# Kernel tuning notes

Hardware: AMD Instinct MI355X
Metric: run time of the kernel (lower is better)

Reference implementation:

```python
import jax, jax.numpy as jnp
import numpy as np

B_GRAPHS, N_NODES = 16, 4096
IN_CH, HID = 256, 512
HEADS, HC = 1, 512  # SGFormerAttention(hidden, heads=1, head_channels=hidden)
NUM_LAYERS = 2
LN_EPS = 1e-5
QK_EPS = 1e-6


def setup_inputs() -> dict:
    key = jax.random.key(0)
    ks = jax.random.split(key, 10)

    def w(k, shape, scale=0.02):
        return jax.random.normal(k, shape, jnp.float32) * scale

    inp = {
        "x": jax.random.normal(ks[0], (B_GRAPHS * N_NODES, IN_CH), jnp.float32),
        "fc0_w": w(ks[1], (HID, IN_CH)),
        "fc0_b": jnp.zeros((HID,), jnp.float32),
        "ln0_g": jnp.ones((HID,), jnp.float32),
        "ln0_b": jnp.zeros((HID,), jnp.float32),
        "q0_w": w(ks[2], (HEADS * HC, HID)),
        "k0_w": w(ks[3], (HEADS * HC, HID)),
        "v0_w": w(ks[4], (HEADS * HC, HID)),
        "ln1_g": jnp.ones((HID,), jnp.float32),
        "ln1_b": jnp.zeros((HID,), jnp.float32),
        "q1_w": w(ks[5], (HEADS * HC, HID)),
        "k1_w": w(ks[6], (HEADS * HC, HID)),
        "v1_w": w(ks[7], (HEADS * HC, HID)),
        "ln2_g": jnp.ones((HID,), jnp.float32),
        "ln2_b": jnp.zeros((HID,), jnp.float32),
        "batch": jnp.repeat(jnp.arange(B_GRAPHS, dtype=jnp.int32), N_NODES),
        "num_graphs": B_GRAPHS,
    }
    return inp


def layernorm(x, g, b):
    mu = x.mean(axis=-1, keepdims=True)
    var = ((x - mu) ** 2).mean(axis=-1, keepdims=True)
    return (x - mu) / jnp.sqrt(var + LN_EPS) * g + b


def sg_attention(x, qw, kw, vw):
    # x: [B, N, HID]; linear (kernelized) global attention, softmax-free.
    B, N, _ = x.shape
    q = (x @ qw.T).reshape(B, N, HEADS, HC)
    k = (x @ kw.T).reshape(B, N, HEADS, HC)
    v = (x @ vw.T).reshape(B, N, HEADS, HC)
    q = jnp.where(q == 0, QK_EPS, q)
    k = jnp.where(k == 0, QK_EPS, k)
    q = q / jnp.linalg.norm(q, axis=-1, keepdims=True)
    k = k / jnp.linalg.norm(k, axis=-1, keepdims=True)
    kvs = jnp.einsum('blhm,blhd->bhmd', k, v)          # [B,H,HC,HC]
    num = jnp.einsum('bnhm,bhmd->bnhd', q, kvs) + N * v
    ks_sum = k.sum(axis=1)                             # [B,H,HC]
    denom = jnp.einsum('bnhm,bhm->bnh', q, ks_sum)[..., None] + float(N)
    return (num / denom).mean(axis=2)                  # [B,N,HC] (mean over heads)


def reference(x, fc0_w, fc0_b, ln0_g, ln0_b,
              q0_w, k0_w, v0_w, ln1_g, ln1_b,
              q1_w, k1_w, v1_w, ln2_g, ln2_b,
              batch, num_graphs):
    total = x.shape[0]
    # stable sort by graph id, remember inverse permutation
    indices = jnp.argsort(batch, stable=True)
    rev_perm = jnp.zeros((total,), jnp.int32).at[indices].set(
        jnp.arange(total, dtype=jnp.int32))
    xs = x[indices]
    # uniform graph sizes -> to_dense_batch is a reshape; mask is all-True
    h = xs.reshape(num_graphs, total // num_graphs, x.shape[1])
    h = h @ fc0_w.T + fc0_b
    h = jax.nn.relu(layernorm(h, ln0_g, ln0_b))  # dropout inactive (eval)
    layers = [h]
    for (qw, kw, vw, g, b) in ((q0_w, k0_w, v0_w, ln1_g, ln1_b),
                               (q1_w, k1_w, v1_w, ln2_g, ln2_b)):
        a = sg_attention(layers[-1], qw, kw, vw)
        a = (a + layers[-1]) / 2.0
        a = jax.nn.relu(layernorm(a, g, b))
        layers.append(a)
    out = layers[-1].reshape(total, -1)
    return out[rev_perm]
```

## Files before the change

kernel.cpp:

```cpp
#include <hip/hip_runtime.h>

#define TNODES 65536
#define NGRAPH 16
#define NNODE  4096
#define INCH   256
#define HID    512

using u16 = unsigned short;
using u32 = unsigned int;
using v8s = __attribute__((ext_vector_type(8))) short;
using v4f = __attribute__((ext_vector_type(4))) float;

__device__ __forceinline__ float bf2f(u16 u) {
    union { u32 i; float f; } v; v.i = ((u32)u) << 16; return v.f;
}
__device__ __forceinline__ u16 f2bf(float f) {
    union { float f; u32 i; } v; v.f = f;
    u32 x = v.i;
    return (u16)((x + 0x7fffu + ((x >> 16) & 1u)) >> 16);
}
__device__ __forceinline__ void up4(uint2 p, float* f) {
    f[0] = __uint_as_float(p.x << 16); f[1] = __uint_as_float(p.x & 0xffff0000u);
    f[2] = __uint_as_float(p.y << 16); f[3] = __uint_as_float(p.y & 0xffff0000u);
}
__device__ __forceinline__ uint2 pk4(float a, float b, float c, float d) {
    uint2 r;
    r.x = (u32)f2bf(a) | ((u32)f2bf(b) << 16);
    r.y = (u32)f2bf(c) | ((u32)f2bf(d) << 16);
    return r;
}

#define MFMA(a, b, c) __builtin_amdgcn_mfma_f32_16x16x32_bf16((a), (b), (c), 0, 0, 0)

#define GLD16(gp, sp) __builtin_amdgcn_global_load_lds( \
    (const __attribute__((address_space(1))) u32*)(const void*)(gp), \
    (__attribute__((address_space(3))) u32*)(void*)(sp), 16, 0, 0)

#define CFENCE() asm volatile("" ::: "memory")

__global__ void k_cvt4(const float* __restrict__ s, u16* __restrict__ d, int n4) {
    for (int i = blockIdx.x * blockDim.x + threadIdx.x; i < n4; i += gridDim.x * blockDim.x) {
        float4 f = ((const float4*)s)[i];
        ((uint2*)d)[i] = pk4(f.x, f.y, f.z, f.w);
    }
}

__global__ void k_zero(float* __restrict__ p, int n) {
    int i = blockIdx.x * 256 + threadIdx.x;
    if (i < n) p[i] = 0.f;
}

__global__ void k_red4(const u16* __restrict__ p, u16* __restrict__ o, int n8) {
    const size_t P = (size_t)NGRAPH * HID * HID;
    for (int i = blockIdx.x * blockDim.x + threadIdx.x; i < n8; i += gridDim.x * blockDim.x) {
        size_t b = (size_t)i * 8;
        float s[8] = {0.f, 0.f, 0.f, 0.f, 0.f, 0.f, 0.f, 0.f};
        #pragma unroll
        for (int ss = 0; ss < 4; ++ss) {
            v8s v = *(const v8s*)(p + ss * P + b);
            const u16* vp = (const u16*)&v;
            #pragma unroll
            for (int j = 0; j < 8; ++j) s[j] += bf2f(vp[j]);
        }
        uint2 lo = pk4(s[0], s[1], s[2], s[3]);
        uint2 hi = pk4(s[4], s[5], s[6], s[7]);
        uint4 w; w.x = lo.x; w.y = lo.y; w.z = hi.x; w.w = hi.y;
        *(uint4*)(o + b) = w;
    }
}

template<int LDK, int KLEN>
__device__ __forceinline__ void gemm_core(const u16* __restrict__ A,
                                          const u16* __restrict__ W,
                                          u16* sA, u16* sW, v4f (&acc)[8][2]) {
    const int t = threadIdx.x, lane = t & 63;
    const int q = lane >> 4, m15 = lane & 15;
    const int w = t >> 6, wr = w >> 2, wc = w & 3;

    #pragma unroll
    for (int n = 0; n < 8; ++n)
        #pragma unroll
        for (int rt = 0; rt < 2; ++rt)
            #pragma unroll
            for (int e = 0; e < 4; ++e) acc[n][rt][e] = 0.f;

    int aoff[2], woff[8];
    #pragma unroll
    for (int rt = 0; rt < 2; ++rt) {
        int r = wr * 32 + rt * 16 + m15;
        aoff[rt] = r * 32 + ((q ^ ((r >> 1) & 3)) * 8);
    }
    #pragma unroll
    for (int n = 0; n < 8; ++n) {
        int r = wc * 128 + n * 16 + m15;
        woff[n] = r * 32 + ((q ^ ((r >> 1) & 3)) * 8);
    }

    auto stage = [&](int k0, int buf) {
        u16* dW = sW + buf * (512 * 32);
        #pragma unroll
        for (int p = 0; p < 4; ++p) {
            int sf = p * 512 + t, row = sf >> 2, sl = sf & 3;
            int gc = k0 + ((sl ^ ((row >> 1) & 3)) * 8);
            GLD16(W + (size_t)row * LDK + gc, dW + sf * 8);
        }
        if (t < 256) {
            int row = t >> 2, sl = t & 3;
            int gc = k0 + ((sl ^ ((row >> 1) & 3)) * 8);
            GLD16(A + (size_t)row * LDK + gc, sA + buf * (64 * 32) + t * 8);
        }
    };

    const int KT = KLEN / 32;
    stage(0, 0);
    stage(32, 1);
    int cur = 0;
    const bool lowt = (t < 256);
    for (int kt = 0; kt < KT; ++kt) {
        if (kt + 1 < KT) {
            if (lowt) asm volatile("s_waitcnt vmcnt(5)" ::: "memory");
            else      asm volatile("s_waitcnt vmcnt(4)" ::: "memory");
        } else {
            asm volatile("s_waitcnt vmcnt(0)" ::: "memory");
        }
        __builtin_amdgcn_s_barrier();
        CFENCE();
        __builtin_amdgcn_sched_barrier(0);
        const u16* cA = sA + cur * (64 * 32);
        const u16* cW = sW + cur * (512 * 32);
        v8s b0 = *(const v8s*)(cA + aoff[0]);
        v8s b1 = *(const v8s*)(cA + aoff[1]);
        #pragma unroll
        for (int n = 0; n < 8; ++n) {
            v8s af = *(const v8s*)(cW + woff[n]);
            acc[n][0] = MFMA(af, b0, acc[n][0]);
            acc[n][1] = MFMA(af, b1, acc[n][1]);
        }
        CFENCE();
        __builtin_amdgcn_s_barrier();
        CFENCE();
        if (kt + 2 < KT) stage((kt + 2) * 32, cur);
        cur ^= 1;
    }
}


__device__ __forceinline__ int tswz(int c) {
    return (((c >> 2) & 3) << 4) ^ ((c & 3) << 3);
}

__launch_bounds__(512, 4)
__global__ void k_fc(const u16* __restrict__ xb, const u16* __restrict__ wb,
                     const float* __restrict__ bias, const float* __restrict__ lg,
                     const float* __restrict__ lb, u16* __restrict__ h) {
    __shared__ u16 sA[2][64 * 32];
    __shared__ u16 sW[2][512 * 32];
    __shared__ float red[2][64][4];
    __shared__ float rowv[2][64];
    const int t = threadIdx.x, lane = t & 63, w = t >> 6;
    const int q = lane >> 4, m15 = lane & 15;
    const int wr = w >> 2, wc = w & 3;
    const int bx = (int)blockIdx.x;
    const int swz = (bx & 7) * ((int)gridDim.x >> 3) + (bx >> 3);
    const int r0 = swz * 64;
    v4f acc[8][2];
    gemm_core<INCH, INCH>(xb + (size_t)r0 * INCH, wb, &sA[0][0], &sW[0][0], acc);

    float sm0 = 0.f, sm1 = 0.f, sq0 = 0.f, sq1 = 0.f;
    #pragma unroll
    for (int n = 0; n < 8; ++n) {
        int c = wc * 128 + n * 16 + q * 4;
        float4 bi = *(const float4*)(bias + c);
        const float* bp = &bi.x;
        #pragma unroll
        for (int rt = 0; rt < 2; ++rt)
            #pragma unroll
            for (int e = 0; e < 4; ++e) {
                float a = acc[n][rt][e] + bp[e];
                acc[n][rt][e] = a;
                if (rt == 0) { sm0 += a; sq0 += a * a; } else { sm1 += a; sq1 += a * a; }
            }
    }
    sm0 += __shfl_xor(sm0, 16); sm0 += __shfl_xor(sm0, 32);
    sq0 += __shfl_xor(sq0, 16); sq0 += __shfl_xor(sq0, 32);
    sm1 += __shfl_xor(sm1, 16); sm1 += __shfl_xor(sm1, 32);
    sq1 += __shfl_xor(sq1, 16); sq1 += __shfl_xor(sq1, 32);
    if (lane < 16) {
        red[0][wr * 32 + m15][wc] = sm0; red[0][wr * 32 + 16 + m15][wc] = sm1;
        red[1][wr * 32 + m15][wc] = sq0; red[1][wr * 32 + 16 + m15][wc] = sq1;
    }
    __syncthreads();
    if (t < 64) {
        float tt = red[0][t][0] + red[0][t][1] + red[0][t][2] + red[0][t][3];
        float t2 = red[1][t][0] + red[1][t][1] + red[1][t][2] + red[1][t][3];
        float mu = tt * (1.f / HID);
        float rs = rsqrtf(t2 * (1.f / HID) - mu * mu + 1e-5f);
        rowv[0][t] = mu; rowv[1][t] = rs;
    }
    __syncthreads();
    #pragma unroll
    for (int n = 0; n < 8; ++n) {
        int c = wc * 128 + n * 16 + q * 4;
        float4 g4 = *(const float4*)(lg + c);
        float4 b4 = *(const float4*)(lb + c);
        #pragma unroll
        for (int rt = 0; rt < 2; ++rt) {
            int row = wr * 32 + rt * 16 + m15;
            float mu = rowv[0][row], rs = rowv[1][row];
            float v0 = (acc[n][rt][0] - mu) * rs * g4.x + b4.x;
            float v1 = (acc[n][rt][1] - mu) * rs * g4.y + b4.y;
            float v2 = (acc[n][rt][2] - mu) * rs * g4.z + b4.z;
            float v3 = (acc[n][rt][3] - mu) * rs * g4.w + b4.w;
            v0 = v0 > 0.f ? v0 : 0.f; v1 = v1 > 0.f ? v1 : 0.f;
            v2 = v2 > 0.f ? v2 : 0.f; v3 = v3 > 0.f ? v3 : 0.f;
            *(uint2*)&h[(size_t)(r0 + row) * HID + c] = pk4(v0, v1, v2, v3);
        }
    }
}

__launch_bounds__(512, 4)
__global__ void k_proj(const u16* __restrict__ hsrc, const u16* __restrict__ wkb,
                       const u16* __restrict__ wvb, u16* __restrict__ kt,
                       u16* __restrict__ vt, float* __restrict__ vo,
                       float* __restrict__ ksum) {
    __shared__ char smem[8192 + 65536 + 1024 + 256];
    u16* sA = (u16*)smem;
    u16* sW = (u16*)(smem + 8192);
    u16* sT = sW;
    float (*red)[4] = (float(*)[4])(smem + 8192 + 65536);
    float* rowv = (float*)(smem + 8192 + 65536 + 1024);
    const int t = threadIdx.x, lane = t & 63, w = t >> 6;
    const int q = lane >> 4, m15 = lane & 15;
    const int wr = w >> 2, wc = w & 3;
    const int bx = (int)blockIdx.x;
    const int swz = (bx & 7) * ((int)gridDim.x >> 3) + (bx >> 3);
    const int r0 = swz * 64;
    const int g = swz >> 6;
    const int lbase = (swz & 63) * 64;
    const int mode = blockIdx.y;
    v4f acc[8][2];
    gemm_core<HID, HID>(hsrc + (size_t)r0 * HID, mode ? wvb : wkb,
                        sA, sW, acc);

    if (mode == 0) {
        float sq0 = 0.f, sq1 = 0.f;
        #pragma unroll
        for (int n = 0; n < 8; ++n)
            #pragma unroll
            for (int rt = 0; rt < 2; ++rt)
                #pragma unroll
                for (int e = 0; e < 4; ++e) {
                    float vv = acc[n][rt][e];
                    if (vv == 0.f) vv = 1e-6f;
                    acc[n][rt][e] = vv;
                    if (rt == 0) sq0 += vv * vv; else sq1 += vv * vv;
                }
        sq0 += __shfl_xor(sq0, 16); sq0 += __shfl_xor(sq0, 32);
        sq1 += __shfl_xor(sq1, 16); sq1 += __shfl_xor(sq1, 32);
        if (lane < 16) {
            red[wr * 32 + m15][wc] = sq0; red[wr * 32 + 16 + m15][wc] = sq1;
        }
        __syncthreads();
        if (t < 64)
            rowv[t] = rsqrtf(red[t][0] + red[t][1] + red[t][2] + red[t][3]);
        __syncthreads();
        #pragma unroll
        for (int n = 0; n < 8; ++n)
            #pragma unroll
            for (int rt = 0; rt < 2; ++rt) {
                int row = wr * 32 + rt * 16 + m15;
                float rn = rowv[row];
                #pragma unroll
                for (int e = 0; e < 4; ++e) {
                    int c = wc * 128 + n * 16 + q * 4 + e;
                    sT[(c << 6) + (row ^ tswz(c))] = f2bf(acc[n][rt][e] * rn);
                }
            }
        __syncthreads();
        const int ch = t;
        const int xs = (((ch >> 2) & 3) << 1) ^ (ch & 3);
        u16* op = kt + ((size_t)(g * 512 + ch)) * NNODE + lbase;
        float sum = 0.f;
        #pragma unroll
        for (int jj = 0; jj < 8; ++jj) {
            v8s cvec = *(const v8s*)&sT[(ch << 6) + jj * 8];
            int l0 = (jj ^ xs) * 8;
            *(v8s*)(op + l0) = cvec;
            const u16* cp = (const u16*)&cvec;
            #pragma unroll
            for (int i = 0; i < 8; ++i) sum += bf2f(cp[i]);
        }
        atomicAdd(&ksum[g * 512 + ch], sum);
    } else {
        #pragma unroll
        for (int n = 0; n < 8; ++n) {
            int c = wc * 128 + n * 16 + q * 4;
            #pragma unroll
            for (int rt = 0; rt < 2; ++rt) {
                int row = wr * 32 + rt * 16 + m15;
                float4 o = {acc[n][rt][0], acc[n][rt][1], acc[n][rt][2], acc[n][rt][3]};
                *(float4*)&vo[(size_t)(r0 + row) * HID + c] = o;
                #pragma unroll
                for (int e = 0; e < 4; ++e)
                    sT[((c + e) << 6) + (row ^ tswz(c + e))] = f2bf(acc[n][rt][e]);
            }
        }
        __syncthreads();
        const int ch = t;
        const int xs = (((ch >> 2) & 3) << 1) ^ (ch & 3);
        u16* op = vt + ((size_t)(g * 512 + ch)) * NNODE + lbase;
        #pragma unroll
        for (int jj = 0; jj < 8; ++jj) {
            v8s cvec = *(const v8s*)&sT[(ch << 6) + jj * 8];
            int l0 = (jj ^ xs) * 8;
            *(v8s*)(op + l0) = cvec;
        }
    }
}

__launch_bounds__(512, 4)
__global__ void k_kvmm2(const u16* __restrict__ kt, const u16* __restrict__ vt,
                        u16* __restrict__ kvp) {
    __shared__ u16 sA[2][64 * 32];
    __shared__ u16 sW[2][512 * 32];
    const int t = threadIdx.x, lane = t & 63, w = t >> 6;
    const int q = lane >> 4, m15 = lane & 15;
    const int wr = w >> 2, wc = w & 3;
    const int bx = (int)blockIdx.x;
    const int swz = (bx & 7) * 64 + (bx >> 3);
    const int db = swz & 7, s = (swz >> 3) & 3, g = swz >> 5;
    const u16* A = vt + ((size_t)(g * 512 + db * 64)) * NNODE + s * 1024;
    const u16* W = kt + ((size_t)(g * 512)) * NNODE + s * 1024;
    v4f acc[8][2];
    gemm_core<NNODE, 1024>(A, W, &sA[0][0], &sW[0][0], acc);
    u16* plane = kvp + (size_t)s * NGRAPH * HID * HID;
    #pragma unroll
    for (int n = 0; n < 8; ++n) {
        int m = wc * 128 + n * 16 + q * 4;
        #pragma unroll
        for (int rt = 0; rt < 2; ++rt) {
            int d = db * 64 + wr * 32 + rt * 16 + m15;
            *(uint2*)&plane[((size_t)(g * 512) + d) * 512 + m] =
                pk4(acc[n][rt][0], acc[n][rt][1], acc[n][rt][2], acc[n][rt][3]);
        }
    }
}

__launch_bounds__(512, 4)
__global__ void k_qnorm(const u16* __restrict__ hsrc, const u16* __restrict__ qwb,
                        const float* __restrict__ ks, u16* __restrict__ qo,
                        float* __restrict__ dnv) {
    __shared__ u16 sA[2][64 * 32];
    __shared__ u16 sW[2][512 * 32];
    __shared__ float red[2][64][4];
    __shared__ float rowv[64];
    const int t = threadIdx.x, lane = t & 63, w = t >> 6;
    const int q = lane >> 4, m15 = lane & 15;
    const int wr = w >> 2, wc = w & 3;
    const int bx = (int)blockIdx.x;
    const int swz = (bx & 7) * ((int)gridDim.x >> 3) + (bx >> 3);
    const int r0 = swz * 64;
    const int gi = swz >> 6;
    v4f acc[8][2];
    gemm_core<HID, HID>(hsrc + (size_t)r0 * HID, qwb, &sA[0][0], &sW[0][0], acc);

    float ss0 = 0.f, ss1 = 0.f, ws0 = 0.f, ws1 = 0.f;
    #pragma unroll
    for (int n = 0; n < 8; ++n) {
        int c = wc * 128 + n * 16 + q * 4;
        float4 kv = *(const float4*)(ks + (gi << 9) + c);
        const float* kp = &kv.x;
        #pragma unroll
        for (int rt = 0; rt < 2; ++rt)
            #pragma unroll
            for (int e = 0; e < 4; ++e) {
                float vv = acc[n][rt][e];
                if (vv == 0.f) vv = 1e-6f;
                acc[n][rt][e] = vv;
                if (rt == 0) { ss0 += vv * vv; ws0 += vv * kp[e]; }
                else         { ss1 += vv * vv; ws1 += vv * kp[e]; }
            }
    }
    ss0 += __shfl_xor(ss0, 16); ss0 += __shfl_xor(ss0, 32);
    ss1 += __shfl_xor(ss1, 16); ss1 += __shfl_xor(ss1, 32);
    ws0 += __shfl_xor(ws0, 16); ws0 += __shfl_xor(ws0, 32);
    ws1 += __shfl_xor(ws1, 16); ws1 += __shfl_xor(ws1, 32);
    if (lane < 16) {
        red[0][wr * 32 + m15][wc] = ss0; red[0][wr * 32 + 16 + m15][wc] = ss1;
        red[1][wr * 32 + m15][wc] = ws0; red[1][wr * 32 + 16 + m15][wc] = ws1;
    }
    __syncthreads();
    if (t < 64) {
        float st = red[0][t][0] + red[0][t][1] + red[0][t][2] + red[0][t][3];
        float wt = red[1][t][0] + red[1][t][1] + red[1][t][2] + red[1][t][3];
        float rn = rsqrtf(st);
        rowv[t] = rn;
        dnv[r0 + t] = 1.f / (rn * wt + (float)NNODE);
    }
    __syncthreads();
    #pragma unroll
    for (int n = 0; n < 8; ++n) {
        int c = wc * 128 + n * 16 + q * 4;
        #pragma unroll
        for (int rt = 0; rt < 2; ++rt) {
            int row = wr * 32 + rt * 16 + m15;
            float rn = rowv[row];
            *(uint2*)&qo[(size_t)(r0 + row) * HID + c] =
                pk4(acc[n][rt][0] * rn, acc[n][rt][1] * rn,
                    acc[n][rt][2] * rn, acc[n][rt][3] * rn);
        }
    }
}

__launch_bounds__(512, 4)
__global__ void k_attn2(const u16* __restrict__ qhat, const u16* __restrict__ kvstb,
                        const float* __restrict__ dnv, const float* __restrict__ vsrc,
                        const u16* __restrict__ hsrc, const float* __restrict__ lg,
                        const float* __restrict__ lb, u16* __restrict__ outb,
                        float* __restrict__ outf) {
    __shared__ u16 sA[2][64 * 32];
    __shared__ u16 sW[2][512 * 32];
    __shared__ float red[2][64][4];
    __shared__ float rowv[2][64];
    const int t = threadIdx.x, lane = t & 63, w = t >> 6;
    const int q = lane >> 4, m15 = lane & 15;
    const int wr = w >> 2, wc = w & 3;
    const int bx = (int)blockIdx.x;
    const int swz = (bx & 7) * ((int)gridDim.x >> 3) + (bx >> 3);
    const int r0 = swz * 64;
    const int gi = swz >> 6;
    v4f acc[8][2];
    gemm_core<HID, HID>(qhat + (size_t)r0 * HID, kvstb + (size_t)gi * HID * HID,
                        &sA[0][0], &sW[0][0], acc);

    const float dv0 = dnv[r0 + wr * 32 + m15];
    const float dv1 = dnv[r0 + wr * 32 + 16 + m15];
    float sm0 = 0.f, sm1 = 0.f, sq0 = 0.f, sq1 = 0.f;
    #pragma unroll
    for (int n = 0; n < 8; ++n) {
        int c = wc * 128 + n * 16 + q * 4;
        #pragma unroll
        for (int rt = 0; rt < 2; ++rt) {
            int row = wr * 32 + rt * 16 + m15;
            size_t og = (size_t)(r0 + row) * HID + c;
            float hh[4]; up4(*(const uint2*)&hsrc[og], hh);
            float4 vv = *(const float4*)&vsrc[og];
            const float* vp = &vv.x;
            float dv = rt ? dv1 : dv0;
            #pragma unroll
            for (int e = 0; e < 4; ++e) {
                float a = ((acc[n][rt][e] + (float)NNODE * vp[e]) * dv + hh[e]) * 0.5f;
                acc[n][rt][e] = a;
                if (rt == 0) { sm0 += a; sq0 += a * a; } else { sm1 += a; sq1 += a * a; }
            }
        }
    }
    sm0 += __shfl_xor(sm0, 16); sm0 += __shfl_xor(sm0, 32);
    sq0 += __shfl_xor(sq0, 16); sq0 += __shfl_xor(sq0, 32);
    sm1 += __shfl_xor(sm1, 16); sm1 += __shfl_xor(sm1, 32);
    sq1 += __shfl_xor(sq1, 16); sq1 += __shfl_xor(sq1, 32);
    if (lane < 16) {
        red[0][wr * 32 + m15][wc] = sm0; red[0][wr * 32 + 16 + m15][wc] = sm1;
        red[1][wr * 32 + m15][wc] = sq0; red[1][wr * 32 + 16 + m15][wc] = sq1;
    }
    __syncthreads();
    if (t < 64) {
        float tt = red[0][t][0] + red[0][t][1] + red[0][t][2] + red[0][t][3];
        float t2 = red[1][t][0] + red[1][t][1] + red[1][t][2] + red[1][t][3];
        float mu = tt * (1.f / HID);
        float rs = rsqrtf(t2 * (1.f / HID) - mu * mu + 1e-5f);
        rowv[0][t] = mu; rowv[1][t] = rs;
    }
    __syncthreads();
    #pragma unroll
    for (int n = 0; n < 8; ++n) {
        int c = wc * 128 + n * 16 + q * 4;
        float4 g4 = *(const float4*)(lg + c);
        float4 b4 = *(const float4*)(lb + c);
        #pragma unroll
        for (int rt = 0; rt < 2; ++rt) {
            int row = wr * 32 + rt * 16 + m15;
            float mu = rowv[0][row], rs = rowv[1][row];
            float v0 = (acc[n][rt][0] - mu) * rs * g4.x + b4.x;
            float v1 = (acc[n][rt][1] - mu) * rs * g4.y + b4.y;
            float v2 = (acc[n][rt][2] - mu) * rs * g4.z + b4.z;
            float v3 = (acc[n][rt][3] - mu) * rs * g4.w + b4.w;
            v0 = v0 > 0.f ? v0 : 0.f; v1 = v1 > 0.f ? v1 : 0.f;
            v2 = v2 > 0.f ? v2 : 0.f; v3 = v3 > 0.f ? v3 : 0.f;
            size_t og = (size_t)(r0 + row) * HID + c;
            if (outf) {
                float4 o = {v0, v1, v2, v3};
                *(float4*)&outf[og] = o;
            } else {
                *(uint2*)&outb[og] = pk4(v0, v1, v2, v3);
            }
        }
    }
}

extern "C" void kernel_launch(void* const* d_in, const int* in_sizes, int n_in,
                              void* d_out, int out_size, void* d_ws, size_t ws_size,
                              hipStream_t stream) {
    const float* x    = (const float*)d_in[0];
    const float* fc0w = (const float*)d_in[1];
    const float* fc0b = (const float*)d_in[2];
    const float* ln0g = (const float*)d_in[3];
    const float* ln0b = (const float*)d_in[4];
    const float* q0w  = (const float*)d_in[5];
    const float* k0w  = (const float*)d_in[6];
    const float* v0w  = (const float*)d_in[7];
    const float* ln1g = (const float*)d_in[8];
    const float* ln1b = (const float*)d_in[9];
    const float* q1w  = (const float*)d_in[10];
    const float* k1w  = (const float*)d_in[11];
    const float* v1w  = (const float*)d_in[12];
    const float* ln2g = (const float*)d_in[13];
    const float* ln2b = (const float*)d_in[14];

    const size_t M64 = (size_t)TNODES * HID * 2;
    const size_t PL  = (size_t)NGRAPH * HID * HID * 2;
    char* wsc = (char*)d_ws;
    u16*   H   = (u16*)wsc;
    u16*   Kt  = (u16*)(wsc + M64);
    u16*   Vt  = (u16*)(wsc + 2 * M64);
    u16*   KVp = (u16*)(wsc + 3 * M64);
    u16*   KVb = (u16*)(wsc + 3 * M64 + 4 * PL);
    float* KS  = (float*)(wsc + 3 * M64 + 5 * PL);
    float* DNV = KS + NGRAPH * HID;
    u16*   Wc  = (u16*)((char*)DNV + (size_t)TNODES * sizeof(float));
    u16* fc0wb = Wc;
    u16* q0b = Wc + 131072;
    u16* k0b = Wc + 393216;
    u16* v0b = Wc + 655360;
    u16* q1b = Wc + 917504;
    u16* k1b = Wc + 1179648;
    u16* v1b = Wc + 1441792;
    u16* Xb  = Vt;
    u16* QH  = Vt;
    float* V = (float*)d_out;

    dim3 b256(256), b512(512);
    k_cvt4<<<dim3(64),  b256, 0, stream>>>(fc0w, fc0wb, HID * INCH / 4);
    k_cvt4<<<dim3(64),  b256, 0, stream>>>(q0w, q0b, HID * HID / 4);
    k_cvt4<<<dim3(64),  b256, 0, stream>>>(k0w, k0b, HID * HID / 4);
    k_cvt4<<<dim3(64),  b256, 0, stream>>>(v0w, v0b, HID * HID / 4);
    k_cvt4<<<dim3(64),  b256, 0, stream>>>(q1w, q1b, HID * HID / 4);
    k_cvt4<<<dim3(64),  b256, 0, stream>>>(k1w, k1b, HID * HID / 4);
    k_cvt4<<<dim3(64),  b256, 0, stream>>>(v1w, v1b, HID * HID / 4);
    k_cvt4<<<dim3(1024), b256, 0, stream>>>(x, Xb, TNODES * INCH / 4);

    k_fc<<<dim3(TNODES / 64), b512, 0, stream>>>(Xb, fc0wb, fc0b, ln0g, ln0b, H);

    k_zero<<<dim3(32), b256, 0, stream>>>(KS, NGRAPH * HID);
    k_proj<<<dim3(TNODES / 64, 2), b512, 0, stream>>>(H, k0b, v0b, Kt, Vt, V, KS);
    k_kvmm2<<<dim3(512), b512, 0, stream>>>(Kt, Vt, KVp);
    k_red4<<<dim3(2048), b256, 0, stream>>>(KVp, KVb, NGRAPH * HID * HID / 8);
    k_qnorm<<<dim3(TNODES / 64), b512, 0, stream>>>(H, q0b, KS, QH, DNV);
    k_attn2<<<dim3(TNODES / 64), b512, 0, stream>>>(QH, KVb, DNV, V, H, ln1g, ln1b,
                                                    H, nullptr);

    k_zero<<<dim3(32), b256, 0, stream>>>(KS, NGRAPH * HID);
    k_proj<<<dim3(TNODES / 64, 2), b512, 0, stream>>>(H, k1b, v1b, Kt, Vt, V, KS);
    k_kvmm2<<<dim3(512), b512, 0, stream>>>(Kt, Vt, KVp);
    k_red4<<<dim3(2048), b256, 0, stream>>>(KVp, KVb, NGRAPH * HID * HID / 8);
    k_qnorm<<<dim3(TNODES / 64), b512, 0, stream>>>(H, q1b, KS, QH, DNV);
    k_attn2<<<dim3(TNODES / 64), b512, 0, stream>>>(QH, KVb, DNV, V, H, ln2g, ln2b,
                                                    nullptr, (float*)d_out);
}
```

Measured before the change: 1.095 ms.

## Enlarge GEMM row tile from 64 to 128 rows across all fused kernels

```diff
diff --git a/kernel.cpp b/kernel.cpp
--- a/kernel.cpp
+++ b/kernel.cpp
@@ -72,7 +72,7 @@
 template<int LDK, int KLEN>
 __device__ __forceinline__ void gemm_core(const u16* __restrict__ A,
                                           const u16* __restrict__ W,
-                                          u16* sA, u16* sW, v4f (&acc)[8][2]) {
+                                          u16* sA, u16* sW, v4f (&acc)[8][4]) {
     const int t = threadIdx.x, lane = t & 63;
     const int q = lane >> 4, m15 = lane & 15;
     const int w = t >> 6, wr = w >> 2, wc = w & 3;
@@ -80,14 +80,14 @@
     #pragma unroll
     for (int n = 0; n < 8; ++n)
         #pragma unroll
-        for (int rt = 0; rt < 2; ++rt)
+        for (int rt = 0; rt < 4; ++rt)
             #pragma unroll
             for (int e = 0; e < 4; ++e) acc[n][rt][e] = 0.f;
 
-    int aoff[2], woff[8];
-    #pragma unroll
-    for (int rt = 0; rt < 2; ++rt) {
-        int r = wr * 32 + rt * 16 + m15;
+    int aoff[4], woff[8];
+    #pragma unroll
+    for (int rt = 0; rt < 4; ++rt) {
+        int r = wr * 64 + rt * 16 + m15;
         aoff[rt] = r * 32 + ((q ^ ((r >> 1) & 3)) * 8);
     }
     #pragma unroll
@@ -104,10 +104,10 @@
             int gc = k0 + ((sl ^ ((row >> 1) & 3)) * 8);
             GLD16(W + (size_t)row * LDK + gc, dW + sf * 8);
         }
-        if (t < 256) {
+        {
             int row = t >> 2, sl = t & 3;
             int gc = k0 + ((sl ^ ((row >> 1) & 3)) * 8);
-            GLD16(A + (size_t)row * LDK + gc, sA + buf * (64 * 32) + t * 8);
+            GLD16(A + (size_t)row * LDK + gc, sA + buf * (128 * 32) + t * 8);
         }
     };
 
@@ -115,26 +115,23 @@
     stage(0, 0);
     stage(32, 1);
     int cur = 0;
-    const bool lowt = (t < 256);
     for (int kt = 0; kt < KT; ++kt) {
-        if (kt + 1 < KT) {
-            if (lowt) asm volatile("s_waitcnt vmcnt(5)" ::: "memory");
-            else      asm volatile("s_waitcnt vmcnt(4)" ::: "memory");
-        } else {
-            asm volatile("s_waitcnt vmcnt(0)" ::: "memory");
-        }
+        if (kt + 1 < KT) asm volatile("s_waitcnt vmcnt(5)" ::: "memory");
+        else             asm volatile("s_waitcnt vmcnt(0)" ::: "memory");
         __builtin_amdgcn_s_barrier();
         CFENCE();
         __builtin_amdgcn_sched_barrier(0);
-        const u16* cA = sA + cur * (64 * 32);
+        const u16* cA = sA + cur * (128 * 32);
         const u16* cW = sW + cur * (512 * 32);
-        v8s b0 = *(const v8s*)(cA + aoff[0]);
-        v8s b1 = *(const v8s*)(cA + aoff[1]);
+        v8s b[4];
+        #pragma unroll
+        for (int rt = 0; rt < 4; ++rt) b[rt] = *(const v8s*)(cA + aoff[rt]);
         #pragma unroll
         for (int n = 0; n < 8; ++n) {
             v8s af = *(const v8s*)(cW + woff[n]);
-            acc[n][0] = MFMA(af, b0, acc[n][0]);
-            acc[n][1] = MFMA(af, b1, acc[n][1]);
+            #pragma unroll
+            for (int rt = 0; rt < 4; ++rt)
+                acc[n][rt] = MFMA(af, b[rt], acc[n][rt]);
         }
         CFENCE();
         __builtin_amdgcn_s_barrier();
@@ -149,48 +146,51 @@
     return (((c >> 2) & 3) << 4) ^ ((c & 3) << 3);
 }
 
-__launch_bounds__(512, 4)
+__launch_bounds__(512, 2)
 __global__ void k_fc(const u16* __restrict__ xb, const u16* __restrict__ wb,
                      const float* __restrict__ bias, const float* __restrict__ lg,
                      const float* __restrict__ lb, u16* __restrict__ h) {
-    __shared__ u16 sA[2][64 * 32];
+    __shared__ u16 sA[2][128 * 32];
     __shared__ u16 sW[2][512 * 32];
-    __shared__ float red[2][64][4];
-    __shared__ float rowv[2][64];
+    __shared__ float red[2][128][4];
+    __shared__ float rowv[2][128];
     const int t = threadIdx.x, lane = t & 63, w = t >> 6;
     const int q = lane >> 4, m15 = lane & 15;
     const int wr = w >> 2, wc = w & 3;
     const int bx = (int)blockIdx.x;
     const int swz = (bx & 7) * ((int)gridDim.x >> 3) + (bx >> 3);
-    const int r0 = swz * 64;
-    v4f acc[8][2];
+    const int r0 = swz * 128;
+    v4f acc[8][4];
     gemm_core<INCH, INCH>(xb + (size_t)r0 * INCH, wb, &sA[0][0], &sW[0][0], acc);
 
-    float sm0 = 0.f, sm1 = 0.f, sq0 = 0.f, sq1 = 0.f;
+    float sm[4] = {0.f, 0.f, 0.f, 0.f}, sq[4] = {0.f, 0.f, 0.f, 0.f};
     #pragma unroll
     for (int n = 0; n < 8; ++n) {
         int c = wc * 128 + n * 16 + q * 4;
         float4 bi = *(const float4*)(bias + c);
         const float* bp = &bi.x;
         #pragma unroll
-        for (int rt = 0; rt < 2; ++rt)
+        for (int rt = 0; rt < 4; ++rt)
             #pragma unroll
             for (int e = 0; e < 4; ++e) {
                 float a = acc[n][rt][e] + bp[e];
                 acc[n][rt][e] = a;
-                if (rt == 0) { sm0 += a; sq0 += a * a; } else { sm1 += a; sq1 += a * a; }
-            }
-    }
-    sm0 += __shfl_xor(sm0, 16); sm0 += __shfl_xor(sm0, 32);
-    sq0 += __shfl_xor(sq0, 16); sq0 += __shfl_xor(sq0, 32);
-    sm1 += __shfl_xor(sm1, 16); sm1 += __shfl_xor(sm1, 32);
-    sq1 += __shfl_xor(sq1, 16); sq1 += __shfl_xor(sq1, 32);
-    if (lane < 16) {
-        red[0][wr * 32 + m15][wc] = sm0; red[0][wr * 32 + 16 + m15][wc] = sm1;
-        red[1][wr * 32 + m15][wc] = sq0; red[1][wr * 32 + 16 + m15][wc] = sq1;
-    }
+                sm[rt] += a; sq[rt] += a * a;
+            }
+    }
+    #pragma unroll
+    for (int rt = 0; rt < 4; ++rt) {
+        sm[rt] += __shfl_xor(sm[rt], 16); sm[rt] += __shfl_xor(sm[rt], 32);
+        sq[rt] += __shfl_xor(sq[rt], 16); sq[rt] += __shfl_xor(sq[rt], 32);
+    }
+    if (lane < 16)
+        #pragma unroll
+        for (int rt = 0; rt < 4; ++rt) {
+            red[0][wr * 64 + rt * 16 + m15][wc] = sm[rt];
+            red[1][wr * 64 + rt * 16 + m15][wc] = sq[rt];
+        }
     __syncthreads();
-    if (t < 64) {
+    if (t < 128) {
         float tt = red[0][t][0] + red[0][t][1] + red[0][t][2] + red[0][t][3];
         float t2 = red[1][t][0] + red[1][t][1] + red[1][t][2] + red[1][t][3];
         float mu = tt * (1.f / HID);
@@ -204,8 +204,8 @@
         float4 g4 = *(const float4*)(lg + c);
         float4 b4 = *(const float4*)(lb + c);
         #pragma unroll
-        for (int rt = 0; rt < 2; ++rt) {
-            int row = wr * 32 + rt * 16 + m15;
+        for (int rt = 0; rt < 4; ++rt) {
+            int row = wr * 64 + rt * 16 + m15;
             float mu = rowv[0][row], rs = rowv[1][row];
             float v0 = (acc[n][rt][0] - mu) * rs * g4.x + b4.x;
             float v1 = (acc[n][rt][1] - mu) * rs * g4.y + b4.y;
@@ -218,77 +218,85 @@
     }
 }
 
-__launch_bounds__(512, 4)
+__launch_bounds__(512, 2)
 __global__ void k_proj(const u16* __restrict__ hsrc, const u16* __restrict__ wkb,
                        const u16* __restrict__ wvb, u16* __restrict__ kt,
                        u16* __restrict__ vt, float* __restrict__ vo,
                        float* __restrict__ ksum) {
-    __shared__ char smem[8192 + 65536 + 1024 + 256];
-    u16* sA = (u16*)smem;
-    u16* sW = (u16*)(smem + 8192);
-    u16* sT = sW;
-    float (*red)[4] = (float(*)[4])(smem + 8192 + 65536);
-    float* rowv = (float*)(smem + 8192 + 65536 + 1024);
+    __shared__ u16 sA[2][128 * 32];
+    __shared__ u16 sW[2][512 * 32];
+    __shared__ float red[128][4];
+    __shared__ float rowv[128];
+    u16* sT = &sW[0][0];
     const int t = threadIdx.x, lane = t & 63, w = t >> 6;
     const int q = lane >> 4, m15 = lane & 15;
     const int wr = w >> 2, wc = w & 3;
     const int bx = (int)blockIdx.x;
     const int swz = (bx & 7) * ((int)gridDim.x >> 3) + (bx >> 3);
-    const int r0 = swz * 64;
-    const int g = swz >> 6;
-    const int lbase = (swz & 63) * 64;
+    const int r0 = swz * 128;
+    const int g = swz >> 5;
+    const int lbase = (swz & 31) * 128;
     const int mode = blockIdx.y;
-    v4f acc[8][2];
+    v4f acc[8][4];
     gemm_core<HID, HID>(hsrc + (size_t)r0 * HID, mode ? wvb : wkb,
-                        sA, sW, acc);
-
+                        &sA[0][0], &sW[0][0], acc);
+
+    const int ch = t;
+    const int xs = (((ch >> 2) & 3) << 1) ^ (ch & 3);
     if (mode == 0) {
-        float sq0 = 0.f, sq1 = 0.f;
+        float sq[4] = {0.f, 0.f, 0.f, 0.f};
         #pragma unroll
         for (int n = 0; n < 8; ++n)
             #pragma unroll
-            for (int rt = 0; rt < 2; ++rt)
+            for (int rt = 0; rt < 4; ++rt)
                 #pragma unroll
                 for (int e = 0; e < 4; ++e) {
                     float vv = acc[n][rt][e];
                     if (vv == 0.f) vv = 1e-6f;
                     acc[n][rt][e] = vv;
-                    if (rt == 0) sq0 += vv * vv; else sq1 += vv * vv;
+                    sq[rt] += vv * vv;
                 }
-        sq0 += __shfl_xor(sq0, 16); sq0 += __shfl_xor(sq0, 32);
-        sq1 += __shfl_xor(sq1, 16); sq1 += __shfl_xor(sq1, 32);
-        if (lane < 16) {
-            red[wr * 32 + m15][wc] = sq0; red[wr * 32 + 16 + m15][wc] = sq1;
-        }
+        #pragma unroll
+        for (int rt = 0; rt < 4; ++rt) {
+            sq[rt] += __shfl_xor(sq[rt], 16); sq[rt] += __shfl_xor(sq[rt], 32);
+        }
+        if (lane < 16)
+            #pragma unroll
+            for (int rt = 0; rt < 4; ++rt)
+                red[wr * 64 + rt * 16 + m15][wc] = sq[rt];
         __syncthreads();
-        if (t < 64)
+        if (t < 128)
             rowv[t] = rsqrtf(red[t][0] + red[t][1] + red[t][2] + red[t][3]);
         __syncthreads();
-        #pragma unroll
-        for (int n = 0; n < 8; ++n)
-            #pragma unroll
-            for (int rt = 0; rt < 2; ++rt) {
-                int row = wr * 32 + rt * 16 + m15;
-                float rn = rowv[row];
+        float sum = 0.f;
+        #pragma unroll
+        for (int pass = 0; pass < 2; ++pass) {
+            if (wr == pass) {
                 #pragma unroll
-                for (int e = 0; e < 4; ++e) {
-                    int c = wc * 128 + n * 16 + q * 4 + e;
-                    sT[(c << 6) + (row ^ tswz(c))] = f2bf(acc[n][rt][e] * rn);
-                }
-            }
-        __syncthreads();
-        const int ch = t;
-        const int xs = (((ch >> 2) & 3) << 1) ^ (ch & 3);
-        u16* op = kt + ((size_t)(g * 512 + ch)) * NNODE + lbase;
-        float sum = 0.f;
-        #pragma unroll
-        for (int jj = 0; jj < 8; ++jj) {
-            v8s cvec = *(const v8s*)&sT[(ch << 6) + jj * 8];
-            int l0 = (jj ^ xs) * 8;
-            *(v8s*)(op + l0) = cvec;
-            const u16* cp = (const u16*)&cvec;
-            #pragma unroll
-            for (int i = 0; i < 8; ++i) sum += bf2f(cp[i]);
+                for (int n = 0; n < 8; ++n)
+                    #pragma unroll
+                    for (int rt = 0; rt < 4; ++rt) {
+                        int rl = rt * 16 + m15;
+                        float rn = rowv[wr * 64 + rl];
+                        #pragma unroll
+                        for (int e = 0; e < 4; ++e) {
+                            int c = wc * 128 + n * 16 + q * 4 + e;
+                            sT[(c << 6) + (rl ^ tswz(c))] = f2bf(acc[n][rt][e] * rn);
+                        }
+                    }
+            }
+            __syncthreads();
+            u16* op = kt + ((size_t)(g * 512 + ch)) * NNODE + lbase + pass * 64;
+            #pragma unroll
+            for (int jj = 0; jj < 8; ++jj) {
+                v8s cvec = *(const v8s*)&sT[(ch << 6) + jj * 8];
+                int l0 = (jj ^ xs) * 8;
+                *(v8s*)(op + l0) = cvec;
+                const u16* cp = (const u16*)&cvec;
+                #pragma unroll
+                for (int i = 0; i < 8; ++i) sum += bf2f(cp[i]);
+            }
+            __syncthreads();
         }
         atomicAdd(&ksum[g * 512 + ch], sum);
     } else {
@@ -296,101 +304,115 @@
         for (int n = 0; n < 8; ++n) {
             int c = wc * 128 + n * 16 + q * 4;
             #pragma unroll
-            for (int rt = 0; rt < 2; ++rt) {
-                int row = wr * 32 + rt * 16 + m15;
+            for (int rt = 0; rt < 4; ++rt) {
+                int row = wr * 64 + rt * 16 + m15;
                 float4 o = {acc[n][rt][0], acc[n][rt][1], acc[n][rt][2], acc[n][rt][3]};
                 *(float4*)&vo[(size_t)(r0 + row) * HID + c] = o;
+            }
+        }
+        #pragma unroll
+        for (int pass = 0; pass < 2; ++pass) {
+            if (wr == pass) {
                 #pragma unroll
-                for (int e = 0; e < 4; ++e)
-                    sT[((c + e) << 6) + (row ^ tswz(c + e))] = f2bf(acc[n][rt][e]);
-            }
-        }
-        __syncthreads();
-        const int ch = t;
-        const int xs = (((ch >> 2) & 3) << 1) ^ (ch & 3);
-        u16* op = vt + ((size_t)(g * 512 + ch)) * NNODE + lbase;
-        #pragma unroll
-        for (int jj = 0; jj < 8; ++jj) {
-            v8s cvec = *(const v8s*)&sT[(ch << 6) + jj * 8];
-            int l0 = (jj ^ xs) * 8;
-            *(v8s*)(op + l0) = cvec;
-        }
-    }
-}
-
-__launch_bounds__(512, 4)
+                for (int n = 0; n < 8; ++n)
+                    #pragma unroll
+                    for (int rt = 0; rt < 4; ++rt) {
+                        int rl = rt * 16 + m15;
+                        #pragma unroll
+                        for (int e = 0; e < 4; ++e) {
+                            int c = wc * 128 + n * 16 + q * 4 + e;
+                            sT[(c << 6) + (rl ^ tswz(c))] = f2bf(acc[n][rt][e]);
+                        }
+                    }
+            }
+            __syncthreads();
+            u16* op = vt + ((size_t)(g * 512 + ch)) * NNODE + lbase + pass * 64;
+            #pragma unroll
+            for (int jj = 0; jj < 8; ++jj) {
+                v8s cvec = *(const v8s*)&sT[(ch << 6) + jj * 8];
+                int l0 = (jj ^ xs) * 8;
+                *(v8s*)(op + l0) = cvec;
+            }
+            __syncthreads();
+        }
+    }
+}
+
+__launch_bounds__(512, 2)
 __global__ void k_kvmm2(const u16* __restrict__ kt, const u16* __restrict__ vt,
                         u16* __restrict__ kvp) {
-    __shared__ u16 sA[2][64 * 32];
+    __shared__ u16 sA[2][128 * 32];
     __shared__ u16 sW[2][512 * 32];
     const int t = threadIdx.x, lane = t & 63, w = t >> 6;
     const int q = lane >> 4, m15 = lane & 15;
     const int wr = w >> 2, wc = w & 3;
     const int bx = (int)blockIdx.x;
-    const int swz = (bx & 7) * 64 + (bx >> 3);
-    const int db = swz & 7, s = (swz >> 3) & 3, g = swz >> 5;
-    const u16* A = vt + ((size_t)(g * 512 + db * 64)) * NNODE + s * 1024;
+    const int swz = (bx & 7) * 32 + (bx >> 3);
+    const int db = swz & 3, s = (swz >> 2) & 3, g = swz >> 4;
+    const u16* A = vt + ((size_t)(g * 512 + db * 128)) * NNODE + s * 1024;
     const u16* W = kt + ((size_t)(g * 512)) * NNODE + s * 1024;
-    v4f acc[8][2];
+    v4f acc[8][4];
     gemm_core<NNODE, 1024>(A, W, &sA[0][0], &sW[0][0], acc);
     u16* plane = kvp + (size_t)s * NGRAPH * HID * HID;
     #pragma unroll
     for (int n = 0; n < 8; ++n) {
         int m = wc * 128 + n * 16 + q * 4;
         #pragma unroll
-        for (int rt = 0; rt < 2; ++rt) {
-            int d = db * 64 + wr * 32 + rt * 16 + m15;
+        for (int rt = 0; rt < 4; ++rt) {
+            int d = db * 128 + wr * 64 + rt * 16 + m15;
             *(uint2*)&plane[((size_t)(g * 512) + d) * 512 + m] =
                 pk4(acc[n][rt][0], acc[n][rt][1], acc[n][rt][2], acc[n][rt][3]);
         }
     }
 }
 
-__launch_bounds__(512, 4)
+__launch_bounds__(512, 2)
 __global__ void k_qnorm(const u16* __restrict__ hsrc, const u16* __restrict__ qwb,
                         const float* __restrict__ ks, u16* __restrict__ qo,
                         float* __restrict__ dnv) {
-    __shared__ u16 sA[2][64 * 32];
+    __shared__ u16 sA[2][128 * 32];
     __shared__ u16 sW[2][512 * 32];
-    __shared__ float red[2][64][4];
-    __shared__ float rowv[64];
+    __shared__ float red[2][128][4];
+    __shared__ float rowv[128];
     const int t = threadIdx.x, lane = t & 63, w = t >> 6;
     const int q = lane >> 4, m15 = lane & 15;
     const int wr = w >> 2, wc = w & 3;
     const int bx = (int)blockIdx.x;
     const int swz = (bx & 7) * ((int)gridDim.x >> 3) + (bx >> 3);
-    const int r0 = swz * 64;
-    const int gi = swz >> 6;
-    v4f acc[8][2];
+    const int r0 = swz * 128;
+    const int gi = swz >> 5;
+    v4f acc[8][4];
     gemm_core<HID, HID>(hsrc + (size_t)r0 * HID, qwb, &sA[0][0], &sW[0][0], acc);
 
-    float ss0 = 0.f, ss1 = 0.f, ws0 = 0.f, ws1 = 0.f;
+    float ss[4] = {0.f, 0.f, 0.f, 0.f}, ws[4] = {0.f, 0.f, 0.f, 0.f};
     #pragma unroll
     for (int n = 0; n < 8; ++n) {
         int c = wc * 128 + n * 16 + q * 4;
         float4 kv = *(const float4*)(ks + (gi << 9) + c);
         const float* kp = &kv.x;
         #pragma unroll
-        for (int rt = 0; rt < 2; ++rt)
+        for (int rt = 0; rt < 4; ++rt)
             #pragma unroll
             for (int e = 0; e < 4; ++e) {
                 float vv = acc[n][rt][e];
                 if (vv == 0.f) vv = 1e-6f;
                 acc[n][rt][e] = vv;
-                if (rt == 0) { ss0 += vv * vv; ws0 += vv * kp[e]; }
-                else         { ss1 += vv * vv; ws1 += vv * kp[e]; }
-            }
-    }
-    ss0 += __shfl_xor(ss0, 16); ss0 += __shfl_xor(ss0, 32);
-    ss1 += __shfl_xor(ss1, 16); ss1 += __shfl_xor(ss1, 32);
-    ws0 += __shfl_xor(ws0, 16); ws0 += __shfl_xor(ws0, 32);
-    ws1 += __shfl_xor(ws1, 16); ws1 += __shfl_xor(ws1, 32);
-    if (lane < 16) {
-        red[0][wr * 32 + m15][wc] = ss0; red[0][wr * 32 + 16 + m15][wc] = ss1;
-        red[1][wr * 32 + m15][wc] = ws0; red[1][wr * 32 + 16 + m15][wc] = ws1;
-    }
+                ss[rt] += vv * vv; ws[rt] += vv * kp[e];
+            }
+    }
+    #pragma unroll
+    for (int rt = 0; rt < 4; ++rt) {
+        ss[rt] += __shfl_xor(ss[rt], 16); ss[rt] += __shfl_xor(ss[rt], 32);
+        ws[rt] += __shfl_xor(ws[rt], 16); ws[rt] += __shfl_xor(ws[rt], 32);
+    }
+    if (lane < 16)
+        #pragma unroll
+        for (int rt = 0; rt < 4; ++rt) {
+            red[0][wr * 64 + rt * 16 + m15][wc] = ss[rt];
+            red[1][wr * 64 + rt * 16 + m15][wc] = ws[rt];
+        }
     __syncthreads();
-    if (t < 64) {
+    if (t < 128) {
         float st = red[0][t][0] + red[0][t][1] + red[0][t][2] + red[0][t][3];
         float wt = red[1][t][0] + red[1][t][1] + red[1][t][2] + red[1][t][3];
         float rn = rsqrtf(st);
@@ -402,8 +424,8 @@
     for (int n = 0; n < 8; ++n) {
         int c = wc * 128 + n * 16 + q * 4;
         #pragma unroll
-        for (int rt = 0; rt < 2; ++rt) {
-            int row = wr * 32 + rt * 16 + m15;
+        for (int rt = 0; rt < 4; ++rt) {
+            int row = wr * 64 + rt * 16 + m15;
             float rn = rowv[row];
             *(uint2*)&qo[(size_t)(r0 + row) * HID + c] =
                 pk4(acc[n][rt][0] * rn, acc[n][rt][1] * rn,
@@ -412,59 +434,62 @@
     }
 }
 
-__launch_bounds__(512, 4)
+__launch_bounds__(512, 2)
 __global__ void k_attn2(const u16* __restrict__ qhat, const u16* __restrict__ kvstb,
                         const float* __restrict__ dnv, const float* __restrict__ vsrc,
                         const u16* __restrict__ hsrc, const float* __restrict__ lg,
                         const float* __restrict__ lb, u16* __restrict__ outb,
                         float* __restrict__ outf) {
-    __shared__ u16 sA[2][64 * 32];
+    __shared__ u16 sA[2][128 * 32];
     __shared__ u16 sW[2][512 * 32];
-    __shared__ float red[2][64][4];
-    __shared__ float rowv[2][64];
+    __shared__ float red[2][128][4];
+    __shared__ float rowv[2][128];
     const int t = threadIdx.x, lane = t & 63, w = t >> 6;
     const int q = lane >> 4, m15 = lane & 15;
     const int wr = w >> 2, wc = w & 3;
     const int bx = (int)blockIdx.x;
     const int swz = (bx & 7) * ((int)gridDim.x >> 3) + (bx >> 3);
-    const int r0 = swz * 64;
-    const int gi = swz >> 6;
-    v4f acc[8][2];
+    const int r0 = swz * 128;
+    const int gi = swz >> 5;
+    v4f acc[8][4];
     gemm_core<HID, HID>(qhat + (size_t)r0 * HID, kvstb + (size_t)gi * HID * HID,
                         &sA[0][0], &sW[0][0], acc);
 
-    const float dv0 = dnv[r0 + wr * 32 + m15];
-    const float dv1 = dnv[r0 + wr * 32 + 16 + m15];
-    float sm0 = 0.f, sm1 = 0.f, sq0 = 0.f, sq1 = 0.f;
+    float dv[4];
+    #pragma unroll
+    for (int rt = 0; rt < 4; ++rt) dv[rt] = dnv[r0 + wr * 64 + rt * 16 + m15];
+    float sm[4] = {0.f, 0.f, 0.f, 0.f}, sq[4] = {0.f, 0.f, 0.f, 0.f};
     #pragma unroll
     for (int n = 0; n < 8; ++n) {
         int c = wc * 128 + n * 16 + q * 4;
         #pragma unroll
-        for (int rt = 0; rt < 2; ++rt) {
-            int row = wr * 32 + rt * 16 + m15;
+        for (int rt = 0; rt < 4; ++rt) {
+            int row = wr * 64 + rt * 16 + m15;
             size_t og = (size_t)(r0 + row) * HID + c;
             float hh[4]; up4(*(const uint2*)&hsrc[og], hh);
             float4 vv = *(const float4*)&vsrc[og];
             const float* vp = &vv.x;
-            float dv = rt ? dv1 : dv0;
             #pragma unroll
             for (int e = 0; e < 4; ++e) {
-                float a = ((acc[n][rt][e] + (float)NNODE * vp[e]) * dv + hh[e]) * 0.5f;
+                float a = ((acc[n][rt][e] + (float)NNODE * vp[e]) * dv[rt] + hh[e]) * 0.5f;
                 acc[n][rt][e] = a;
-                if (rt == 0) { sm0 += a; sq0 += a * a; } else { sm1 += a; sq1 += a * a; }
-            }
-        }
-    }
-    sm0 += __shfl_xor(sm0, 16); sm0 += __shfl_xor(sm0, 32);
-    sq0 += __shfl_xor(sq0, 16); sq0 += __shfl_xor(sq0, 32);
-    sm1 += __shfl_xor(sm1, 16); sm1 += __shfl_xor(sm1, 32);
-    sq1 += __shfl_xor(sq1, 16); sq1 += __shfl_xor(sq1, 32);
-    if (lane < 16) {
-        red[0][wr * 32 + m15][wc] = sm0; red[0][wr * 32 + 16 + m15][wc] = sm1;
-        red[1][wr * 32 + m15][wc] = sq0; red[1][wr * 32 + 16 + m15][wc] = sq1;
-    }
+                sm[rt] += a; sq[rt] += a * a;
+            }
+        }
+    }
+    #pragma unroll
+    for (int rt = 0; rt < 4; ++rt) {
+        sm[rt] += __shfl_xor(sm[rt], 16); sm[rt] += __shfl_xor(sm[rt], 32);
+        sq[rt] += __shfl_xor(sq[rt], 16); sq[rt] += __shfl_xor(sq[rt], 32);
+    }
+    if (lane < 16)
+        #pragma unroll
+        for (int rt = 0; rt < 4; ++rt) {
+            red[0][wr * 64 + rt * 16 + m15][wc] = sm[rt];
+            red[1][wr * 64 + rt * 16 + m15][wc] = sq[rt];
+        }
     __syncthreads();
-    if (t < 64) {
+    if (t < 128) {
         float tt = red[0][t][0] + red[0][t][1] + red[0][t][2] + red[0][t][3];
         float t2 = red[1][t][0] + red[1][t][1] + red[1][t][2] + red[1][t][3];
         float mu = tt * (1.f / HID);
@@ -478,8 +503,8 @@
         float4 g4 = *(const float4*)(lg + c);
         float4 b4 = *(const float4*)(lb + c);
         #pragma unroll
-        for (int rt = 0; rt < 2; ++rt) {
-            int row = wr * 32 + rt * 16 + m15;
+        for (int rt = 0; rt < 4; ++rt) {
+            int row = wr * 64 + rt * 16 + m15;
             float mu = rowv[0][row], rs = rowv[1][row];
             float v0 = (acc[n][rt][0] - mu) * rs * g4.x + b4.x;
             float v1 = (acc[n][rt][1] - mu) * rs * g4.y + b4.y;
@@ -549,21 +574,21 @@
     k_cvt4<<<dim3(64),  b256, 0, stream>>>(v1w, v1b, HID * HID / 4);
     k_cvt4<<<dim3(1024), b256, 0, stream>>>(x, Xb, TNODES * INCH / 4);
 
-    k_fc<<<dim3(TNODES / 64), b512, 0, stream>>>(Xb, fc0wb, fc0b, ln0g, ln0b, H);
+    k_fc<<<dim3(TNODES / 128), b512, 0, stream>>>(Xb, fc0wb, fc0b, ln0g, ln0b, H);
 
     k_zero<<<dim3(32), b256, 0, stream>>>(KS, NGRAPH * HID);
-    k_proj<<<dim3(TNODES / 64, 2), b512, 0, stream>>>(H, k0b, v0b, Kt, Vt, V, KS);
-    k_kvmm2<<<dim3(512), b512, 0, stream>>>(Kt, Vt, KVp);
+    k_proj<<<dim3(TNODES / 128, 2), b512, 0, stream>>>(H, k0b, v0b, Kt, Vt, V, KS);
+    k_kvmm2<<<dim3(256), b512, 0, stream>>>(Kt, Vt, KVp);
     k_red4<<<dim3(2048), b256, 0, stream>>>(KVp, KVb, NGRAPH * HID * HID / 8);
-    k_qnorm<<<dim3(TNODES / 64), b512, 0, stream>>>(H, q0b, KS, QH, DNV);
-    k_attn2<<<dim3(TNODES / 64), b512, 0, stream>>>(QH, KVb, DNV, V, H, ln1g, ln1b,
-                                                    H, nullptr);
+    k_qnorm<<<dim3(TNODES / 128), b512, 0, stream>>>(H, q0b, KS, QH, DNV);
+    k_attn2<<<dim3(TNODES / 128), b512, 0, stream>>>(QH, KVb, DNV, V, H, ln1g, ln1b,
+                                                     H, nullptr);
 
     k_zero<<<dim3(32), b256, 0, stream>>>(KS, NGRAPH * HID);
-    k_proj<<<dim3(TNODES / 64, 2), b512, 0, stream>>>(H, k1b, v1b, Kt, Vt, V, KS);
-    k_kvmm2<<<dim3(512), b512, 0, stream>>>(Kt, Vt, KVp);
+    k_proj<<<dim3(TNODES / 128, 2), b512, 0, stream>>>(H, k1b, v1b, Kt, Vt, V, KS);
+    k_kvmm2<<<dim3(256), b512, 0, stream>>>(Kt, Vt, KVp);
     k_red4<<<dim3(2048), b256, 0, stream>>>(KVp, KVb, NGRAPH * HID * HID / 8);
-    k_qnorm<<<dim3(TNODES / 64), b512, 0, stream>>>(H, q1b, KS, QH, DNV);
-    k_attn2<<<dim3(TNODES / 64), b512, 0, stream>>>(QH, KVb, DNV, V, H, ln2g, ln2b,
-                                                    nullptr, (float*)d_out);
-}
+    k_qnorm<<<dim3(TNODES / 128), b512, 0, stream>>>(H, q1b, KS, QH, DNV);
+    k_attn2<<<dim3(TNODES / 128), b512, 0, stream>>>(QH, KVb, DNV, V, H, ln2g, ln2b,
+                                                     nullptr, (float*)d_out);
+}
```

After: 1.034 ms. 5.6% less time.
